# Performance work log

Hardware: AMD Instinct MI355X
Metric: run time of the kernel (lower is better)

Reference implementation:

```python
import jax, jax.numpy as jnp
import numpy as np

B, K, D_MODEL = 128, 256, 256
NUM_CODES, BASIS_DIM = 1024, 2700


def setup_inputs() -> dict:
    key = jax.random.key(0)
    k1, k2, k3 = jax.random.split(key, 3)
    slot_features = jax.random.normal(k1, (B, K, D_MODEL), dtype=jnp.float32)
    W_proj = jax.random.normal(k2, (BASIS_DIM, D_MODEL), dtype=jnp.float32) * 0.02
    b_proj = jnp.zeros((BASIS_DIM,), dtype=jnp.float32)
    # NMF basis atoms are non-negative
    basis = jax.random.uniform(k3, (NUM_CODES, BASIS_DIM), dtype=jnp.float32)
    return {"slot_features": slot_features, "W_proj": W_proj, "b_proj": b_proj, "basis": basis}


def reference(slot_features, W_proj, b_proj, basis):
    b, k, _ = slot_features.shape
    # slot_proj: Linear(d_model -> basis_dim)
    z_e = jnp.einsum('bkd,ed->bke', slot_features, W_proj) + b_proj  # [B,K,BASIS_DIM]
    z_flat = z_e.reshape(b * k, -1)                                   # [BK, D]
    # squared-euclidean distance to every codebook atom: [BK, NUM_CODES]
    dist = (jnp.sum(z_flat * z_flat, axis=1, keepdims=True)
            - 2.0 * (z_flat @ basis.T)
            + jnp.sum(basis * basis, axis=1)[None, :])
    indices = jnp.argmin(dist, axis=-1)                               # [BK]
    e_i = basis[indices].reshape(b, k, -1)                            # [B,K,D]
    # straight-through: forward value == z_e, grads pass through z_e only
    q_st = z_e + jax.lax.stop_gradient(e_i - z_e)
    commit_loss = jnp.mean((z_e - jax.lax.stop_gradient(e_i)) ** 2)
    vq_loss = 0.25 * commit_loss
    logits = -dist                                                    # [BK, NUM_CODES]
    avg_probs = jnp.mean(jax.nn.softmax(logits, axis=-1), axis=0)     # [NUM_CODES]
    entropy = -jnp.sum(avg_probs * jnp.log(avg_probs + 1e-8))
    return q_st, indices.reshape(b, k), vq_loss, entropy
```

## Files before the change

kernel.cpp:

```cpp
#include <hip/hip_runtime.h>
#include <math.h>

#define ED 2700
#define NC 1024
#define DM 256
#define BKROWS 32768

#define IDX_OFF 88473600
#define VQ_OFF  88506368
#define ENT_OFF 88506369

#define KPAD 2720
#define K2CH 8

typedef float  f32x4  __attribute__((ext_vector_type(4)));
typedef short  bf16x8 __attribute__((ext_vector_type(8)));

__device__ inline unsigned short f2bf(float x) {
    unsigned int u = __float_as_uint(x);
    unsigned int r = (u + 0x7FFFu + ((u >> 16) & 1u)) >> 16;
    return (unsigned short)r;
}
__device__ inline float bf2f(unsigned short h) {
    return __uint_as_float(((unsigned int)h) << 16);
}


__global__ __launch_bounds__(256)
void k_packS(const float* __restrict__ S, unsigned short* __restrict__ Sh,
             unsigned short* __restrict__ Sm) {
    const size_t i4 = (size_t)blockIdx.x * 256 + threadIdx.x;
    const float4 v = *(const float4*)(S + i4 * 4);
    ushort4 hv, mv;
    unsigned short* hp = (unsigned short*)&hv;
    unsigned short* mp = (unsigned short*)&mv;
    const float xs[4] = {v.x, v.y, v.z, v.w};
    #pragma unroll
    for (int j = 0; j < 4; ++j) {
        const unsigned short h = f2bf(xs[j]);
        hp[j] = h;
        mp[j] = f2bf(xs[j] - bf2f(h));
    }
    *(ushort4*)(Sh + i4 * 4) = hv;
    *(ushort4*)(Sm + i4 * 4) = mv;
}

__global__ void k_prepB(const float* __restrict__ basis, const float* __restrict__ bproj,
                        float* __restrict__ bP, float* __restrict__ bsq) {
    const int c = blockIdx.x;
    const int t = threadIdx.x;
    const float* row = basis + (size_t)c * ED;
    float* dst = bP + (size_t)c * KPAD;
    double s2 = 0.0, sp = 0.0;
    for (int j = t; j < ED; j += 256) {
        const float x = row[j];
        dst[j] = x;
        s2 += (double)x * (double)x;
        sp += (double)x * (double)bproj[j];
    }
    if (t < KPAD - ED) dst[ED + t] = 0.f;
    __shared__ double sd[512];
    sd[t] = s2; sd[256 + t] = sp;
    __syncthreads();
    for (int off = 128; off > 0; off >>= 1) {
        if (t < off) { sd[t] += sd[t + off]; sd[256 + t] += sd[256 + t + off]; }
        __syncthreads();
    }
    if (t == 0) bsq[c] = (float)(sd[0] - 2.0 * sd[256]);
}

__global__ __launch_bounds__(256)
void k_padWT(const float* __restrict__ W, float* __restrict__ WT) {
    const int e0 = blockIdx.x * 64;
    const int d0 = blockIdx.y * 64;
    __shared__ float tbuf[64][65];
    const int t  = threadIdx.x;
    const int r  = t >> 2;
    const int q4 = t & 3;
    #pragma unroll
    for (int j = 0; j < 4; ++j) {
        const int col = q4 * 16 + j * 4;
        const int e = e0 + r;
        float4 v = make_float4(0.f, 0.f, 0.f, 0.f);
        if (e < ED) v = *(const float4*)(W + (size_t)e * DM + d0 + col);
        tbuf[r][col + 0] = v.x; tbuf[r][col + 1] = v.y;
        tbuf[r][col + 2] = v.z; tbuf[r][col + 3] = v.w;
    }
    __syncthreads();
    #pragma unroll
    for (int j = 0; j < 4; ++j) {
        const int col = q4 * 16 + j * 4;
        if (e0 + col < KPAD) {
            float4 o;
            o.x = tbuf[col + 0][r]; o.y = tbuf[col + 1][r];
            o.z = tbuf[col + 2][r]; o.w = tbuf[col + 3][r];
            *(float4*)(WT + (size_t)(d0 + r) * KPAD + e0 + col) = o;
        }
    }
}

__global__ __launch_bounds__(256)
void k_uv2(const float* __restrict__ WT, const float* __restrict__ bproj,
           float* __restrict__ uv) {
    const int b = blockIdx.x;
    const int t = threadIdx.x;
    double s = 0.0;
    if (b < 256) {
        const float* row = WT + (size_t)b * KPAD;
        for (int j = t; j < ED; j += 256) s += (double)row[j] * (double)bproj[j];
    } else {
        for (int j = t; j < ED; j += 256) { const double x = bproj[j]; s += x * x; }
    }
    __shared__ double sd[256];
    sd[t] = s;
    __syncthreads();
    for (int off = 128; off > 0; off >>= 1) {
        if (t < off) sd[t] += sd[t + off];
        __syncthreads();
    }
    if (t == 0) uv[b] = (float)sd[0];
}

__global__ __launch_bounds__(256)
void k_colsum(const float* __restrict__ S, float* __restrict__ cspart) {
    const int m0 = blockIdx.x * 256;
    const int t  = threadIdx.x;
    double s = 0.0;
    for (int r = 0; r < 256; ++r) s += (double)S[(size_t)(m0 + r) * DM + t];
    cspart[blockIdx.x * 256 + t] = (float)s;
}

__global__ __launch_bounds__(256)
void k_gsplit(const float* __restrict__ A, const float* __restrict__ B,
              float* __restrict__ Cp, int nld) {
    const int n0  = blockIdx.x * 64;
    const int m0  = blockIdx.y * 64;
    const int k00 = blockIdx.z * 544;
    float* Cout = Cp + (size_t)blockIdx.z * (size_t)gridDim.y * 64 * nld;
    const int t  = threadIdx.x;
    const int tx = t & 15, ty = t >> 4;

    __shared__ float alds[32 * 68];
    __shared__ float blds[32 * 68];

    float acc[4][4] = {};

    for (int k0 = k00; k0 < k00 + 544; k0 += 32) {
        #pragma unroll
        for (int rep = 0; rep < 2; ++rep) {
            const int id  = t + rep * 256;
            const int row = id >> 3, kq = id & 7;
            const float4 va = *(const float4*)(A + (size_t)(m0 + row) * KPAD + k0 + 4 * kq);
            alds[(4*kq+0)*68 + row] = va.x;
            alds[(4*kq+1)*68 + row] = va.y;
            alds[(4*kq+2)*68 + row] = va.z;
            alds[(4*kq+3)*68 + row] = va.w;
            const float4 vb = *(const float4*)(B + (size_t)(n0 + row) * KPAD + k0 + 4 * kq);
            blds[(4*kq+0)*68 + row] = vb.x;
            blds[(4*kq+1)*68 + row] = vb.y;
            blds[(4*kq+2)*68 + row] = vb.z;
            blds[(4*kq+3)*68 + row] = vb.w;
        }
        __syncthreads();
        #pragma unroll 8
        for (int k = 0; k < 32; ++k) {
            const float4 a = *(const float4*)&alds[k*68 + 4*ty];
            const float4 b = *(const float4*)&blds[k*68 + 4*tx];
            const float av[4] = {a.x, a.y, a.z, a.w};
            const float bv[4] = {b.x, b.y, b.z, b.w};
            #pragma unroll
            for (int i = 0; i < 4; ++i)
                #pragma unroll
                for (int j = 0; j < 4; ++j)
                    acc[i][j] = fmaf(av[i], bv[j], acc[i][j]);
        }
        __syncthreads();
    }
    #pragma unroll
    for (int i = 0; i < 4; ++i) {
        float4 o; o.x = acc[i][0]; o.y = acc[i][1]; o.z = acc[i][2]; o.w = acc[i][3];
        *(float4*)(Cout + (size_t)(m0 + 4*ty + i) * nld + n0 + 4*tx) = o;
    }
}

__global__ __launch_bounds__(256)
void k_redP(const float* __restrict__ Pp, unsigned short* __restrict__ Ph,
            unsigned short* __restrict__ Pm) {
    const size_t idx = (size_t)blockIdx.x * 256 + threadIdx.x;
    float s = 0.f;
    #pragma unroll
    for (int k = 0; k < 5; ++k) s += Pp[(size_t)k * 262144 + idx];
    const unsigned short h = f2bf(s);
    Ph[idx] = h;
    Pm[idx] = f2bf(s - bf2f(h));
}

__global__ __launch_bounds__(256)
void k_redM2(const float* __restrict__ Mp, unsigned short* __restrict__ Mh,
             unsigned short* __restrict__ Mm) {
    const size_t idx = (size_t)blockIdx.x * 256 + threadIdx.x;
    float s = 0.f;
    #pragma unroll
    for (int k = 0; k < 5; ++k) s += Mp[(size_t)k * 65536 + idx];
    const unsigned short h = f2bf(s);
    Mh[idx] = h;
    Mm[idx] = f2bf(s - bf2f(h));
}

__global__ __launch_bounds__(512, 2)
void k_gemm2(const unsigned short* __restrict__ Zh, const unsigned short* __restrict__ Zm,
             const unsigned short* __restrict__ Bh, const unsigned short* __restrict__ Bm,
             float* __restrict__ G) {
    __shared__ unsigned short lds[2 * 32768];

    const int bid  = blockIdx.x;
    const int xcd  = bid & 7, local = bid >> 3;
    const int mt   = xcd * 16 + (local >> 2);
    const int nt   = local & 3;
    const int m0   = mt * 256, n0 = nt * 256;
    const int tid  = threadIdx.x;
    const int w    = tid >> 6, l = tid & 63;
    const int wr   = (w >> 2) * 128;
    const int wc   = (w & 3) * 64;
    const int lrow = l & 15;
    const int lu   = l >> 4;

    const unsigned short* hsrc[4][2];
    int hlds[4][2];
    #pragma unroll
    for (int ht = 0; ht < 4; ++ht) {
        #pragma unroll
        for (int j = 0; j < 2; ++j) {
            const int slot = j * 512 + tid;
            const int rwh  = slot >> 3;
            const int unit = slot & 7;
            int row; bool isB;
            if (ht == 0)      { row = (rwh & 63) + (rwh >> 6) * 128;       isB = false; }
            else if (ht == 1) { row = 64 + (rwh & 63) + (rwh >> 6) * 128;  isB = false; }
            else if (ht == 2) { row = (rwh & 31) + (rwh >> 5) * 64;        isB = true;  }
            else              { row = 32 + (rwh & 31) + (rwh >> 5) * 64;   isB = true;  }
            const int sg   = unit ^ (row & 7);
            const int pl   = sg >> 2;
            const int koff = (sg & 3) * 8;
            if (!isB) hsrc[ht][j] = (pl ? Zm : Zh) + (size_t)(m0 + row) * DM + koff;
            else      hsrc[ht][j] = (pl ? Bm : Bh) + (size_t)(n0 + row) * DM + koff;
            hlds[ht][j] = (isB ? 16384 : 0) + row * 64 + unit * 8;
        }
    }

    f32x4 acc[8][4];
    #pragma unroll
    for (int i = 0; i < 8; ++i)
        #pragma unroll
        for (int j = 0; j < 4; ++j) acc[i][j] = (f32x4){0.f, 0.f, 0.f, 0.f};

    #define STAGE_HALF(ht, ck, db) { \
        _Pragma("unroll") \
        for (int j = 0; j < 2; ++j) \
            __builtin_amdgcn_global_load_lds( \
                (const __attribute__((address_space(1))) unsigned int*)(const void*)(hsrc[ht][j] + (ck) * 32), \
                (__attribute__((address_space(3))) unsigned int*)(void*)&lds[(db) * 32768 + hlds[ht][j]], \
                16, 0, 0); \
    }

    #define LOAD_A(db, qm) { \
        const unsigned short* At = &lds[(db) * 32768]; \
        _Pragma("unroll") \
        for (int f = 0; f < 4; ++f) { \
            const int row = wr + ((qm) * 4 + f) * 16 + lrow; \
            ah[f] = *(const bf16x8*)(At + row * 64 + (((0 + lu) ^ (row & 7))) * 8); \
            am[f] = *(const bf16x8*)(At + row * 64 + (((4 + lu) ^ (row & 7))) * 8); \
        } \
    }
    #define LOAD_B(db, qn) { \
        const unsigned short* Bt = &lds[(db) * 32768 + 16384]; \
        _Pragma("unroll") \
        for (int f = 0; f < 2; ++f) { \
            const int col = wc + ((qn) * 2 + f) * 16 + lrow; \
            bh[f] = *(const bf16x8*)(Bt + col * 64 + (((0 + lu) ^ (col & 7))) * 8); \
            bm[f] = *(const bf16x8*)(Bt + col * 64 + (((4 + lu) ^ (col & 7))) * 8); \
        } \
    }
    #define MFMA_Q(qm, qn) { \
        __builtin_amdgcn_s_setprio(1); \
        _Pragma("unroll") \
        for (int i = 0; i < 4; ++i) \
            _Pragma("unroll") \
            for (int j = 0; j < 2; ++j) { \
                f32x4 cc = acc[(qm) * 4 + i][(qn) * 2 + j]; \
                cc = __builtin_amdgcn_mfma_f32_16x16x32_bf16(ah[i], bh[j], cc, 0, 0, 0); \
                cc = __builtin_amdgcn_mfma_f32_16x16x32_bf16(ah[i], bm[j], cc, 0, 0, 0); \
                cc = __builtin_amdgcn_mfma_f32_16x16x32_bf16(am[i], bh[j], cc, 0, 0, 0); \
                acc[(qm) * 4 + i][(qn) * 2 + j] = cc; \
            } \
        __builtin_amdgcn_s_setprio(0); \
    }
    #define VM8  asm volatile("s_waitcnt vmcnt(8)" ::: "memory");
    #define BAR  __builtin_amdgcn_s_barrier();

    STAGE_HALF(0, 0, 0) STAGE_HALF(2, 0, 0) STAGE_HALF(3, 0, 0) STAGE_HALF(1, 0, 0)
    STAGE_HALF(0, 1, 1) STAGE_HALF(2, 1, 1)
    VM8
    BAR

    for (int c = 0; c < K2CH - 2; ++c) {
        const int cb = c & 1, ob = cb ^ 1;
        bf16x8 ah[4], am[4], bh[2], bm[2];
        LOAD_A(cb, 0) LOAD_B(cb, 0)
        STAGE_HALF(3, c + 1, ob)
        BAR
        MFMA_Q(0, 0)
        VM8
        BAR
        LOAD_B(cb, 1)
        STAGE_HALF(1, c + 1, ob)
        BAR
        MFMA_Q(0, 1)
        VM8
        BAR
        LOAD_A(cb, 1) LOAD_B(cb, 0)
        STAGE_HALF(0, c + 2, cb)
        BAR
        MFMA_Q(1, 0)
        BAR
        LOAD_B(cb, 1)
        STAGE_HALF(2, c + 2, cb)
        BAR
        MFMA_Q(1, 1)
        VM8
        BAR
    }

    STAGE_HALF(3, K2CH - 1, (K2CH - 1) & 1) STAGE_HALF(1, K2CH - 1, (K2CH - 1) & 1)
    asm volatile("s_waitcnt vmcnt(0)" ::: "memory");
    BAR
    #pragma unroll
    for (int e = 0; e < 2; ++e) {
        const int cb = (K2CH - 2 + e) & 1;
        bf16x8 ah[4], am[4], bh[2], bm[2];
        LOAD_A(cb, 0) LOAD_B(cb, 0)
        MFMA_Q(0, 0)
        LOAD_B(cb, 1)
        MFMA_Q(0, 1)
        LOAD_A(cb, 1) LOAD_B(cb, 0)
        MFMA_Q(1, 0)
        LOAD_B(cb, 1)
        MFMA_Q(1, 1)
    }

    #pragma unroll
    for (int fm = 0; fm < 8; ++fm)
        #pragma unroll
        for (int fn = 0; fn < 4; ++fn) {
            const int col = n0 + wc + fn * 16 + lrow;
            #pragma unroll
            for (int r = 0; r < 4; ++r) {
                const int row = m0 + wr + fm * 16 + lu * 4 + r;
                G[(size_t)row * NC + col] = acc[fm][fn][r];
            }
        }
}

__global__ __launch_bounds__(512, 2)
void k_ydot(const unsigned short* __restrict__ Zh, const unsigned short* __restrict__ Zm,
            const unsigned short* __restrict__ Bh, const unsigned short* __restrict__ Bm,
            const float* __restrict__ S, float* __restrict__ ydotpart) {
    __shared__ unsigned short lds[2 * 32768];

    const int bid  = blockIdx.x;
    const int xcd  = bid & 7, local = bid >> 3;
    const int mt   = xcd * 16 + local;
    const int m0   = mt * 256, n0 = 0;
    const int tid  = threadIdx.x;
    const int w    = tid >> 6, l = tid & 63;
    const int wr   = (w >> 2) * 128;
    const int wc   = (w & 3) * 64;
    const int lrow = l & 15;
    const int lu   = l >> 4;

    const unsigned short* hsrc[4][2];
    int hlds[4][2];
    #pragma unroll
    for (int ht = 0; ht < 4; ++ht) {
        #pragma unroll
        for (int j = 0; j < 2; ++j) {
            const int slot = j * 512 + tid;
            const int rwh  = slot >> 3;
            const int unit = slot & 7;
            int row; bool isB;
            if (ht == 0)      { row = (rwh & 63) + (rwh >> 6) * 128;       isB = false; }
            else if (ht == 1) { row = 64 + (rwh & 63) + (rwh >> 6) * 128;  isB = false; }
            else if (ht == 2) { row = (rwh & 31) + (rwh >> 5) * 64;        isB = true;  }
            else              { row = 32 + (rwh & 31) + (rwh >> 5) * 64;   isB = true;  }
            const int sg   = unit ^ (row & 7);
            const int pl   = sg >> 2;
            const int koff = (sg & 3) * 8;
            if (!isB) hsrc[ht][j] = (pl ? Zm : Zh) + (size_t)(m0 + row) * DM + koff;
            else      hsrc[ht][j] = (pl ? Bm : Bh) + (size_t)(n0 + row) * DM + koff;
            hlds[ht][j] = (isB ? 16384 : 0) + row * 64 + unit * 8;
        }
    }

    f32x4 acc[8][4];
    #pragma unroll
    for (int i = 0; i < 8; ++i)
        #pragma unroll
        for (int j = 0; j < 4; ++j) acc[i][j] = (f32x4){0.f, 0.f, 0.f, 0.f};

    STAGE_HALF(0, 0, 0) STAGE_HALF(2, 0, 0) STAGE_HALF(3, 0, 0) STAGE_HALF(1, 0, 0)
    STAGE_HALF(0, 1, 1) STAGE_HALF(2, 1, 1)
    VM8
    BAR

    for (int c = 0; c < K2CH - 2; ++c) {
        const int cb = c & 1, ob = cb ^ 1;
        bf16x8 ah[4], am[4], bh[2], bm[2];
        LOAD_A(cb, 0) LOAD_B(cb, 0)
        STAGE_HALF(3, c + 1, ob)
        BAR
        MFMA_Q(0, 0)
        VM8
        BAR
        LOAD_B(cb, 1)
        STAGE_HALF(1, c + 1, ob)
        BAR
        MFMA_Q(0, 1)
        VM8
        BAR
        LOAD_A(cb, 1) LOAD_B(cb, 0)
        STAGE_HALF(0, c + 2, cb)
        BAR
        MFMA_Q(1, 0)
        BAR
        LOAD_B(cb, 1)
        STAGE_HALF(2, c + 2, cb)
        BAR
        MFMA_Q(1, 1)
        VM8
        BAR
    }

    STAGE_HALF(3, K2CH - 1, (K2CH - 1) & 1) STAGE_HALF(1, K2CH - 1, (K2CH - 1) & 1)
    asm volatile("s_waitcnt vmcnt(0)" ::: "memory");
    BAR
    #pragma unroll
    for (int e = 0; e < 2; ++e) {
        const int cb = (K2CH - 2 + e) & 1;
        bf16x8 ah[4], am[4], bh[2], bm[2];
        LOAD_A(cb, 0) LOAD_B(cb, 0)
        MFMA_Q(0, 0)
        LOAD_B(cb, 1)
        MFMA_Q(0, 1)
        LOAD_A(cb, 1) LOAD_B(cb, 0)
        MFMA_Q(1, 0)
        LOAD_B(cb, 1)
        MFMA_Q(1, 1)
    }
    #undef STAGE_HALF
    #undef LOAD_A
    #undef LOAD_B
    #undef MFMA_Q
    #undef VM8
    #undef BAR

    float part = 0.f;
    #pragma unroll
    for (int fm = 0; fm < 8; ++fm)
        #pragma unroll
        for (int fn = 0; fn < 4; ++fn) {
            const int col = wc + fn * 16 + lrow;
            #pragma unroll
            for (int r = 0; r < 4; ++r) {
                const int row = m0 + wr + fm * 16 + lu * 4 + r;
                part += acc[fm][fn][r] * S[(size_t)row * DM + col];
            }
        }
    __syncthreads();
    float* red = (float*)lds;
    red[tid] = part;
    __syncthreads();
    for (int off = 256; off > 0; off >>= 1) {
        if (tid < off) red[tid] += red[tid + off];
        __syncthreads();
    }
    if (tid == 0) ydotpart[bid] = red[0];
}

__global__ __launch_bounds__(512)
void k_post(const float* __restrict__ G, const float* __restrict__ bsq,
            float* __restrict__ A, float* __restrict__ wgpart,
            int* __restrict__ idxws, float* __restrict__ out) {
    const int bid = blockIdx.x;
    const int wr0 = bid * 32;
    const int t   = threadIdx.x;
    const int cg  = t & 127;
    const int rq  = t >> 7;
    const int r0  = rq * 8;
    const int c0  = cg * 4;
    const int c1  = 512 + cg * 4;

    __shared__ float sm[9280];
    float* red_v    = sm;
    int*   red_i    = (int*)(sm + 4096);
    float* row_dmin = sm + 8192;
    float* row_s    = sm + 8224;
    float* pc       = sm + 8256;

    float acc[8][8];
    #pragma unroll
    for (int i = 0; i < 8; ++i) {
        const float4 g0 = *(const float4*)&G[(size_t)(wr0 + r0 + i) * NC + c0];
        const float4 g1 = *(const float4*)&G[(size_t)(wr0 + r0 + i) * NC + c1];
        acc[i][0] = g0.x; acc[i][1] = g0.y; acc[i][2] = g0.z; acc[i][3] = g0.w;
        acc[i][4] = g1.x; acc[i][5] = g1.y; acc[i][6] = g1.z; acc[i][7] = g1.w;
    }

    float bsqv[8];
    #pragma unroll
    for (int j = 0; j < 4; ++j) { bsqv[j] = bsq[c0 + j]; bsqv[4 + j] = bsq[c1 + j]; }

    #pragma unroll
    for (int i = 0; i < 8; ++i)
        #pragma unroll
        for (int j = 0; j < 8; ++j)
            acc[i][j] = bsqv[j] - 2.f * acc[i][j];

    #pragma unroll
    for (int i = 0; i < 8; ++i) {
        float bv = acc[i][0]; int bi = c0;
        #pragma unroll
        for (int j = 1; j < 8; ++j) {
            const int c = (j < 4) ? (c0 + j) : (c1 + (j - 4));
            if (acc[i][j] < bv || (acc[i][j] == bv && c < bi)) { bv = acc[i][j]; bi = c; }
        }
        red_v[(r0 + i) * 128 + cg] = bv;
        red_i[(r0 + i) * 128 + cg] = bi;
    }
    __syncthreads();
    if (t < 32) {
        float bv = red_v[t * 128]; int bi = red_i[t * 128];
        for (int x = 1; x < 128; ++x) {
            const float v = red_v[t * 128 + x];
            const int  iv = red_i[t * 128 + x];
            if (v < bv || (v == bv && iv < bi)) { bv = v; bi = iv; }
        }
        row_dmin[t] = bv;
        idxws[wr0 + t] = bi;
        out[IDX_OFF + wr0 + t] = (float)bi;
    }
    __syncthreads();

    float su[8];
    #pragma unroll
    for (int i = 0; i < 8; ++i) {
        const float dm = row_dmin[r0 + i];
        float s = 0.f;
        #pragma unroll
        for (int j = 0; j < 8; ++j) {
            const float u = expf(dm - acc[i][j]);
            acc[i][j] = u;
            s += u;
        }
        su[i] = s;
    }
    #pragma unroll
    for (int i = 0; i < 8; ++i) red_v[(r0 + i) * 128 + cg] = su[i];
    __syncthreads();
    if (t < 32) {
        float s = 0.f;
        for (int x = 0; x < 128; ++x) s += red_v[t * 128 + x];
        row_s[t] = s;
    }
    __syncthreads();

    float rcp[8];
    #pragma unroll
    for (int i = 0; i < 8; ++i) rcp[i] = 1.f / row_s[r0 + i];

    pc[t] = 0.f; pc[t + 512] = 0.f;
    __syncthreads();
    #pragma unroll
    for (int j = 0; j < 8; ++j) {
        const int c = (j < 4) ? (c0 + j) : (c1 + (j - 4));
        float s = 0.f;
        #pragma unroll
        for (int i = 0; i < 8; ++i) s += acc[i][j] * rcp[i];
        atomicAdd(&pc[c], s);
    }
    __syncthreads();
    atomicAdd(&A[t],       pc[t]);
    atomicAdd(&A[t + 512], pc[t + 512]);

    if (t == 0) {
        float s = 0.f;
        for (int r = 0; r < 32; ++r) s += row_dmin[r];
        wgpart[bid] = s;
    }
}

__global__ void k_final2(const float* __restrict__ wgpart, const float* __restrict__ Aq,
                         const float* __restrict__ ydotpart, const float* __restrict__ cspart,
                         const float* __restrict__ uv, float* __restrict__ out) {
    __shared__ double sd[1024];
    const int t = threadIdx.x;
    sd[t] = (double)wgpart[t];
    __syncthreads();
    for (int off = 512; off > 0; off >>= 1) {
        if (t < off) sd[t] += sd[t + off];
        __syncthreads();
    }
    const double smin = sd[0];
    __syncthreads();
    sd[t] = (t < 128) ? (double)ydotpart[t] : 0.0;
    __syncthreads();
    for (int off = 512; off > 0; off >>= 1) {
        if (t < off) sd[t] += sd[t + off];
        __syncthreads();
    }
    const double sy = sd[0];
    __syncthreads();
    double cu = 0.0;
    if (t < 256) {
        double cs = 0.0;
        for (int b = 0; b < 128; ++b) cs += (double)cspart[b * 256 + t];
        cu = cs * (double)uv[t];
    }
    sd[t] = cu;
    __syncthreads();
    for (int off = 512; off > 0; off >>= 1) {
        if (t < off) sd[t] += sd[t + off];
        __syncthreads();
    }
    if (t == 0) {
        const double szsq = sy + 2.0 * sd[0] + 32768.0 * (double)uv[256];
        out[VQ_OFF] = (float)(0.25 * (smin + szsq) / 88473600.0);
    }
    __syncthreads();
    const double p = (double)Aq[t] * (1.0 / 32768.0);
    sd[t] = -p * log(p + 1e-8);
    __syncthreads();
    for (int off = 512; off > 0; off >>= 1) {
        if (t < off) sd[t] += sd[t + off];
        __syncthreads();
    }
    if (t == 0) out[ENT_OFF] = (float)sd[0];
}

__global__ void k_gather(const float* __restrict__ basis, const int* __restrict__ idxws,
                         float* __restrict__ out) {
    const int r = blockIdx.x;
    const int idx = idxws[r];
    const float4* src = (const float4*)(basis + (size_t)idx * ED);
    float4* dst = (float4*)(out + (size_t)r * ED);
    for (int j = threadIdx.x; j < ED / 4; j += 256) dst[j] = src[j];
}


__global__ void k_bsq(const float* __restrict__ basis, float* __restrict__ bsq) {
    int c = blockIdx.x;
    const float* row = basis + (size_t)c * ED;
    double s = 0.0;
    for (int j = threadIdx.x; j < ED; j += 256) { float v = row[j]; s += (double)v * (double)v; }
    __shared__ double sd[256];
    sd[threadIdx.x] = s;
    __syncthreads();
    for (int off = 128; off > 0; off >>= 1) {
        if (threadIdx.x < off) sd[threadIdx.x] += sd[threadIdx.x + off];
        __syncthreads();
    }
    if (threadIdx.x == 0) bsq[c] = (float)sd[0];
}

__global__ __launch_bounds__(256, 4)
void k_gemm1(const float* __restrict__ S, const float* __restrict__ W,
             const float* __restrict__ bproj, float* __restrict__ Z) {
    const int e0 = blockIdx.x * 64;
    const int m0 = blockIdx.y * 64;
    const int t  = threadIdx.x;
    const int tx = t & 15, ty = t >> 4;
    __shared__ float alds[32 * 68];
    __shared__ float blds[32 * 68];
    float acc[4][4] = {};
    for (int k0 = 0; k0 < DM; k0 += 32) {
        #pragma unroll
        for (int rep = 0; rep < 2; ++rep) {
            const int id  = t + rep * 256;
            const int row = id >> 3, kq = id & 7;
            const float4 va = *(const float4*)(S + (size_t)(m0 + row) * DM + k0 + 4 * kq);
            alds[(4*kq+0)*68 + row] = va.x;
            alds[(4*kq+1)*68 + row] = va.y;
            alds[(4*kq+2)*68 + row] = va.z;
            alds[(4*kq+3)*68 + row] = va.w;
            float4 vb = make_float4(0.f, 0.f, 0.f, 0.f);
            if (e0 + row < ED)
                vb = *(const float4*)(W + (size_t)(e0 + row) * DM + k0 + 4 * kq);
            blds[(4*kq+0)*68 + row] = vb.x;
            blds[(4*kq+1)*68 + row] = vb.y;
            blds[(4*kq+2)*68 + row] = vb.z;
            blds[(4*kq+3)*68 + row] = vb.w;
        }
        __syncthreads();
        #pragma unroll 8
        for (int k = 0; k < 32; ++k) {
            const float4 a = *(const float4*)&alds[k*68 + 4*ty];
            const float4 b = *(const float4*)&blds[k*68 + 4*tx];
            const float av[4] = {a.x, a.y, a.z, a.w};
            const float bv[4] = {b.x, b.y, b.z, b.w};
            #pragma unroll
            for (int i = 0; i < 4; ++i)
                #pragma unroll
                for (int j = 0; j < 4; ++j)
                    acc[i][j] = fmaf(av[i], bv[j], acc[i][j]);
        }
        __syncthreads();
    }
    const bool valid = (e0 + 4*tx + 4) <= ED;
    float4 bias = make_float4(0.f, 0.f, 0.f, 0.f);
    if (valid) bias = *(const float4*)(bproj + e0 + 4*tx);
    #pragma unroll
    for (int i = 0; i < 4; ++i) {
        if (valid) {
            float4 o;
            o.x = acc[i][0] + bias.x;
            o.y = acc[i][1] + bias.y;
            o.z = acc[i][2] + bias.z;
            o.w = acc[i][3] + bias.w;
            *(float4*)(Z + (size_t)(m0 + 4*ty + i) * ED + e0 + 4*tx) = o;
        }
    }
}

__global__ __launch_bounds__(64)
void k_zsq(const float* __restrict__ Z, float* __restrict__ zsq) {
    const int r = blockIdx.x;
    const float4* row4 = (const float4*)(Z + (size_t)r * ED);
    double s = 0.0;
    for (int q = threadIdx.x; q < ED / 4; q += 64) {
        const float4 v = row4[q];
        s += (double)v.x * v.x + (double)v.y * v.y + (double)v.z * v.z + (double)v.w * v.w;
    }
    #pragma unroll
    for (int off = 32; off > 0; off >>= 1) s += __shfl_down(s, off);
    if (threadIdx.x == 0) zsq[r] = (float)s;
}

__global__ __launch_bounds__(512, 2)
void k_dist(const float* __restrict__ Z, const float* __restrict__ basis,
            const float* __restrict__ bsq, const float* __restrict__ zsq,
            float* __restrict__ A, float* __restrict__ wgpart,
            int* __restrict__ idxws, float* __restrict__ out) {
    const int bid = blockIdx.x;
    const int wr0 = bid * 32;
    const int t   = threadIdx.x;
    const int cg  = t & 127;
    const int rq  = t >> 7;
    const int r0  = rq * 8;
    const int c0  = cg * 4;
    const int c1  = 512 + cg * 4;
    __shared__ float blds[16 * 1024];
    __shared__ float zlds[16 * 36];
    float acc[8][8];
    #pragma unroll
    for (int i = 0; i < 8; ++i)
        #pragma unroll
        for (int j = 0; j < 8; ++j) acc[i][j] = 0.f;
    for (int k0 = 0; k0 < ED; k0 += 16) {
        const bool full = (k0 + 16) <= ED;
        #pragma unroll
        for (int rep = 0; rep < 2; ++rep) {
            const int c = t + rep * 512;
            const float* bp = basis + (size_t)c * ED + k0;
            if (full) {
                const float4 v0 = *(const float4*)(bp + 0);
                const float4 v1 = *(const float4*)(bp + 4);
                const float4 v2 = *(const float4*)(bp + 8);
                const float4 v3 = *(const float4*)(bp + 12);
                blds[ 0*1024+c]=v0.x; blds[ 1*1024+c]=v0.y; blds[ 2*1024+c]=v0.z; blds[ 3*1024+c]=v0.w;
                blds[ 4*1024+c]=v1.x; blds[ 5*1024+c]=v1.y; blds[ 6*1024+c]=v1.z; blds[ 7*1024+c]=v1.w;
                blds[ 8*1024+c]=v2.x; blds[ 9*1024+c]=v2.y; blds[10*1024+c]=v2.z; blds[11*1024+c]=v2.w;
                blds[12*1024+c]=v3.x; blds[13*1024+c]=v3.y; blds[14*1024+c]=v3.z; blds[15*1024+c]=v3.w;
            } else {
                for (int kk = 0; kk < 16; ++kk)
                    blds[kk*1024 + c] = (k0 + kk < ED) ? bp[kk] : 0.f;
            }
        }
        if (t < 128) {
            const int row = t >> 2, kq = t & 3;
            const float* zp = Z + (size_t)(wr0 + row) * ED + k0 + 4 * kq;
            if (full) {
                const float4 v = *(const float4*)zp;
                zlds[(4*kq+0)*36 + row] = v.x;
                zlds[(4*kq+1)*36 + row] = v.y;
                zlds[(4*kq+2)*36 + row] = v.z;
                zlds[(4*kq+3)*36 + row] = v.w;
            } else {
                for (int j = 0; j < 4; ++j) {
                    const int k = k0 + 4*kq + j;
                    zlds[(4*kq+j)*36 + row] = (k < ED) ? zp[j] : 0.f;
                }
            }
        }
        __syncthreads();
        #pragma unroll
        for (int k = 0; k < 16; ++k) {
            const float4 z0 = *(const float4*)&zlds[k*36 + r0];
            const float4 z1 = *(const float4*)&zlds[k*36 + r0 + 4];
            const float4 b0 = *(const float4*)&blds[k*1024 + c0];
            const float4 b1 = *(const float4*)&blds[k*1024 + c1];
            const float zz[8] = {z0.x, z0.y, z0.z, z0.w, z1.x, z1.y, z1.z, z1.w};
            const float bb[8] = {b0.x, b0.y, b0.z, b0.w, b1.x, b1.y, b1.z, b1.w};
            #pragma unroll
            for (int i = 0; i < 8; ++i)
                #pragma unroll
                for (int j = 0; j < 8; ++j)
                    acc[i][j] = fmaf(zz[i], bb[j], acc[i][j]);
        }
        __syncthreads();
    }
    float* red_v    = blds;
    int*   red_i    = (int*)(blds + 4096);
    float* row_dmin = blds + 8192;
    float* row_s    = blds + 8224;
    float* pc       = blds + 8256;
    float bsqv[8], zsqv[8];
    #pragma unroll
    for (int j = 0; j < 4; ++j) { bsqv[j] = bsq[c0 + j]; bsqv[4 + j] = bsq[c1 + j]; }
    #pragma unroll
    for (int i = 0; i < 8; ++i) zsqv[i] = zsq[wr0 + r0 + i];
    #pragma unroll
    for (int i = 0; i < 8; ++i)
        #pragma unroll
        for (int j = 0; j < 8; ++j) {
            const float tv = zsqv[i] - 2.f * acc[i][j];
            acc[i][j] = tv + bsqv[j];
        }
    #pragma unroll
    for (int i = 0; i < 8; ++i) {
        float bv = acc[i][0]; int bi = c0;
        #pragma unroll
        for (int j = 1; j < 8; ++j) {
            const int c = (j < 4) ? (c0 + j) : (c1 + (j - 4));
            if (acc[i][j] < bv || (acc[i][j] == bv && c < bi)) { bv = acc[i][j]; bi = c; }
        }
        red_v[(r0 + i) * 128 + cg] = bv;
        red_i[(r0 + i) * 128 + cg] = bi;
    }
    __syncthreads();
    if (t < 32) {
        float bv = red_v[t * 128]; int bi = red_i[t * 128];
        for (int x = 1; x < 128; ++x) {
            const float v = red_v[t * 128 + x];
            const int  iv = red_i[t * 128 + x];
            if (v < bv || (v == bv && iv < bi)) { bv = v; bi = iv; }
        }
        row_dmin[t] = bv;
        idxws[wr0 + t] = bi;
        out[IDX_OFF + wr0 + t] = (float)bi;
    }
    __syncthreads();
    float su[8];
    #pragma unroll
    for (int i = 0; i < 8; ++i) {
        const float dm = row_dmin[r0 + i];
        float s = 0.f;
        #pragma unroll
        for (int j = 0; j < 8; ++j) {
            const float u = expf(dm - acc[i][j]);
            acc[i][j] = u;
            s += u;
        }
        su[i] = s;
    }
    #pragma unroll
    for (int i = 0; i < 8; ++i) red_v[(r0 + i) * 128 + cg] = su[i];
    __syncthreads();
    if (t < 32) {
        float s = 0.f;
        for (int x = 0; x < 128; ++x) s += red_v[t * 128 + x];
        row_s[t] = s;
    }
    __syncthreads();
    float rcp[8];
    #pragma unroll
    for (int i = 0; i < 8; ++i) rcp[i] = 1.f / row_s[r0 + i];
    pc[t] = 0.f; pc[t + 512] = 0.f;
    __syncthreads();
    #pragma unroll
    for (int j = 0; j < 8; ++j) {
        const int c = (j < 4) ? (c0 + j) : (c1 + (j - 4));
        float s = 0.f;
        #pragma unroll
        for (int i = 0; i < 8; ++i) s += acc[i][j] * rcp[i];
        atomicAdd(&pc[c], s);
    }
    __syncthreads();
    atomicAdd(&A[t],       pc[t]);
    atomicAdd(&A[t + 512], pc[t + 512]);
    if (t == 0) {
        float s = 0.f;
        for (int r = 0; r < 32; ++r) s += row_dmin[r];
        wgpart[bid] = s;
    }
}

__global__ void k_final(const float* __restrict__ wgpart, const float* __restrict__ A,
                        float* __restrict__ out) {
    __shared__ double sd[1024];
    const int t = threadIdx.x;
    sd[t] = (double)wgpart[t];
    __syncthreads();
    for (int off = 512; off > 0; off >>= 1) {
        if (t < off) sd[t] += sd[t + off];
        __syncthreads();
    }
    if (t == 0) out[VQ_OFF] = (float)(0.25 * sd[0] / 88473600.0);
    __syncthreads();
    const double p = (double)A[t] * (1.0 / 32768.0);
    sd[t] = -p * log(p + 1e-8);
    __syncthreads();
    for (int off = 512; off > 0; off >>= 1) {
        if (t < off) sd[t] += sd[t + off];
        __syncthreads();
    }
    if (t == 0) out[ENT_OFF] = (float)sd[0];
}


extern "C" void kernel_launch(void* const* d_in, const int* in_sizes, int n_in,
                              void* d_out, int out_size, void* d_ws, size_t ws_size,
                              hipStream_t stream) {
    const float* S     = (const float*)d_in[0];
    const float* W     = (const float*)d_in[1];
    const float* bproj = (const float*)d_in[2];
    const float* basis = (const float*)d_in[3];
    float* out = (float*)d_out;
    float* ws  = (float*)d_ws;

    const size_t NEED = (size_t)33951232 * sizeof(float);
    if (ws_size >= NEED) {
        float* A        = ws;
        float* bsq      = ws + 1024;
        float* wgpart   = ws + 2048;
        int*   idxws    = (int*)(ws + 3072);
        float* uv       = ws + 35840;
        float* ydotpart = ws + 36224;
        float* cspart   = ws + 36352;
        unsigned short* Ph = (unsigned short*)(ws + 69120);
        unsigned short* Pm = (unsigned short*)(ws + 200192);
        unsigned short* Mh = (unsigned short*)(ws + 331264);
        unsigned short* Mm = (unsigned short*)(ws + 364032);
        float* G        = ws + 396800;
        float* basisP = G;
        float* WT     = G + 2785280;
        float* Pp     = G + 3481600;
        float* Mp     = G + 4792320;
        unsigned short* Sh = (unsigned short*)out;
        unsigned short* Sm = Sh + (size_t)BKROWS * DM;

        hipMemsetAsync(A, 0, (size_t)NC * sizeof(float), stream);
        k_packS <<<BKROWS * DM / 1024, 256, 0, stream>>>(S, Sh, Sm);
        k_prepB <<<NC, 256, 0, stream>>>(basis, bproj, basisP, bsq);
        k_padWT <<<dim3(43, 4), 256, 0, stream>>>(W, WT);
        k_uv2   <<<257, 256, 0, stream>>>(WT, bproj, uv);
        k_colsum<<<128, 256, 0, stream>>>(S, cspart);
        k_gsplit<<<dim3(4, 16, 5), 256, 0, stream>>>(basisP, WT, Pp, 256);
        k_gsplit<<<dim3(4, 4, 5),  256, 0, stream>>>(WT, WT, Mp, 256);
        k_redP  <<<1024, 256, 0, stream>>>(Pp, Ph, Pm);
        k_redM2 <<<256, 256, 0, stream>>>(Mp, Mh, Mm);
        k_gemm2 <<<512, 512, 0, stream>>>(Sh, Sm, Ph, Pm, G);
        k_ydot  <<<128, 512, 0, stream>>>(Sh, Sm, Mh, Mm, S, ydotpart);
        k_post  <<<BKROWS / 32, 512, 0, stream>>>(G, bsq, A, wgpart, idxws, out);
        k_final2<<<1, 1024, 0, stream>>>(wgpart, A, ydotpart, cspart, uv, out);
        k_gather<<<BKROWS, 256, 0, stream>>>(basis, idxws, out);
    } else {
        float* zsqF    = ws;
        float* A       = ws + 32768;
        float* bsqF    = ws + 33792;
        float* wgpartF = ws + 34816;
        int*   idxwsF  = (int*)(ws + 35840);
        float* Z = out;
        hipMemsetAsync(A, 0, (size_t)NC * sizeof(float), stream);
        k_bsq   <<<NC, 256, 0, stream>>>(basis, bsqF);
        k_gemm1 <<<dim3(43, 512), 256, 0, stream>>>(S, W, bproj, Z);
        k_zsq   <<<BKROWS, 64, 0, stream>>>(Z, zsqF);
        k_dist  <<<BKROWS / 32, 512, 0, stream>>>(Z, basis, bsqF, zsqF, A, wgpartF, idxwsF, out);
        k_final <<<1, 1024, 0, stream>>>(wgpartF, A, out);
        k_gather<<<BKROWS, 256, 0, stream>>>(basis, idxwsF, out);
    }
}
```

Before: 367.6 us.

## Merge prep kernels into one launch and fuse codebook gather into post kernel

Combines the basis prep, W transpose, uv, and column-sum kernels into one multi-role launch. It also merges the two split-K GEMMs and the two reductions into single launches. The gather of selected codebook rows moves into the post/argmin kernel, dropping the index workspace round trip and a separate launch. This cuts launch overhead and lets independent small kernels run concurrently. The cost is that each post block now does extra serial copying, and uv now reads W with strided loads.

```diff
diff --git a/kernel.cpp b/kernel.cpp
--- a/kernel.cpp
+++ b/kernel.cpp
@@ -45,98 +45,108 @@
     *(ushort4*)(Sm + i4 * 4) = mv;
 }
 
-__global__ void k_prepB(const float* __restrict__ basis, const float* __restrict__ bproj,
-                        float* __restrict__ bP, float* __restrict__ bsq) {
-    const int c = blockIdx.x;
-    const int t = threadIdx.x;
-    const float* row = basis + (size_t)c * ED;
-    float* dst = bP + (size_t)c * KPAD;
-    double s2 = 0.0, sp = 0.0;
-    for (int j = t; j < ED; j += 256) {
-        const float x = row[j];
-        dst[j] = x;
-        s2 += (double)x * (double)x;
-        sp += (double)x * (double)bproj[j];
-    }
-    if (t < KPAD - ED) dst[ED + t] = 0.f;
-    __shared__ double sd[512];
-    sd[t] = s2; sd[256 + t] = sp;
-    __syncthreads();
-    for (int off = 128; off > 0; off >>= 1) {
-        if (t < off) { sd[t] += sd[t + off]; sd[256 + t] += sd[256 + t + off]; }
-        __syncthreads();
-    }
-    if (t == 0) bsq[c] = (float)(sd[0] - 2.0 * sd[256]);
-}
-
 __global__ __launch_bounds__(256)
-void k_padWT(const float* __restrict__ W, float* __restrict__ WT) {
-    const int e0 = blockIdx.x * 64;
-    const int d0 = blockIdx.y * 64;
-    __shared__ float tbuf[64][65];
-    const int t  = threadIdx.x;
-    const int r  = t >> 2;
-    const int q4 = t & 3;
-    #pragma unroll
-    for (int j = 0; j < 4; ++j) {
-        const int col = q4 * 16 + j * 4;
-        const int e = e0 + r;
-        float4 v = make_float4(0.f, 0.f, 0.f, 0.f);
-        if (e < ED) v = *(const float4*)(W + (size_t)e * DM + d0 + col);
-        tbuf[r][col + 0] = v.x; tbuf[r][col + 1] = v.y;
-        tbuf[r][col + 2] = v.z; tbuf[r][col + 3] = v.w;
-    }
-    __syncthreads();
-    #pragma unroll
-    for (int j = 0; j < 4; ++j) {
-        const int col = q4 * 16 + j * 4;
-        if (e0 + col < KPAD) {
-            float4 o;
-            o.x = tbuf[col + 0][r]; o.y = tbuf[col + 1][r];
-            o.z = tbuf[col + 2][r]; o.w = tbuf[col + 3][r];
-            *(float4*)(WT + (size_t)(d0 + r) * KPAD + e0 + col) = o;
-        }
-    }
-}
-
-__global__ __launch_bounds__(256)
-void k_uv2(const float* __restrict__ WT, const float* __restrict__ bproj,
-           float* __restrict__ uv) {
+void k_prep1(const float* __restrict__ basis, const float* __restrict__ bproj,
+             const float* __restrict__ W, const float* __restrict__ S,
+             float* __restrict__ bP, float* __restrict__ bsq,
+             float* __restrict__ WT, float* __restrict__ uv,
+             float* __restrict__ cspart) {
+    __shared__ double sdbuf[2080];
     const int b = blockIdx.x;
     const int t = threadIdx.x;
-    double s = 0.0;
-    if (b < 256) {
-        const float* row = WT + (size_t)b * KPAD;
-        for (int j = t; j < ED; j += 256) s += (double)row[j] * (double)bproj[j];
+
+    if (b < 1024) {
+        const int c = b;
+        const float* row = basis + (size_t)c * ED;
+        float* dst = bP + (size_t)c * KPAD;
+        double s2 = 0.0, sp = 0.0;
+        for (int j = t; j < ED; j += 256) {
+            const float x = row[j];
+            dst[j] = x;
+            s2 += (double)x * (double)x;
+            sp += (double)x * (double)bproj[j];
+        }
+        if (t < KPAD - ED) dst[ED + t] = 0.f;
+        double* sd = sdbuf;
+        sd[t] = s2; sd[256 + t] = sp;
+        __syncthreads();
+        for (int off = 128; off > 0; off >>= 1) {
+            if (t < off) { sd[t] += sd[t + off]; sd[256 + t] += sd[256 + t + off]; }
+            __syncthreads();
+        }
+        if (t == 0) bsq[c] = (float)(sd[0] - 2.0 * sd[256]);
+    } else if (b < 1196) {
+        const int i  = b - 1024;
+        const int e0 = (i >> 2) * 64;
+        const int d0 = (i & 3) * 64;
+        float (*tbuf)[65] = (float(*)[65])sdbuf;
+        const int r  = t >> 2;
+        const int q4 = t & 3;
+        #pragma unroll
+        for (int j = 0; j < 4; ++j) {
+            const int col = q4 * 16 + j * 4;
+            const int e = e0 + r;
+            float4 v = make_float4(0.f, 0.f, 0.f, 0.f);
+            if (e < ED) v = *(const float4*)(W + (size_t)e * DM + d0 + col);
+            tbuf[r][col + 0] = v.x; tbuf[r][col + 1] = v.y;
+            tbuf[r][col + 2] = v.z; tbuf[r][col + 3] = v.w;
+        }
+        __syncthreads();
+        #pragma unroll
+        for (int j = 0; j < 4; ++j) {
+            const int col = q4 * 16 + j * 4;
+            if (e0 + col < KPAD) {
+                float4 o;
+                o.x = tbuf[col + 0][r]; o.y = tbuf[col + 1][r];
+                o.z = tbuf[col + 2][r]; o.w = tbuf[col + 3][r];
+                *(float4*)(WT + (size_t)(d0 + r) * KPAD + e0 + col) = o;
+            }
+        }
+    } else if (b < 1453) {
+        const int bb = b - 1196;
+        double s = 0.0;
+        if (bb < 256) {
+            for (int e = t; e < ED; e += 256)
+                s += (double)W[(size_t)e * DM + bb] * (double)bproj[e];
+        } else {
+            for (int j = t; j < ED; j += 256) { const double x = bproj[j]; s += x * x; }
+        }
+        double* sd = sdbuf;
+        sd[t] = s;
+        __syncthreads();
+        for (int off = 128; off > 0; off >>= 1) {
+            if (t < off) sd[t] += sd[t + off];
+            __syncthreads();
+        }
+        if (t == 0) uv[bb] = (float)sd[0];
     } else {
-        for (int j = t; j < ED; j += 256) { const double x = bproj[j]; s += x * x; }
-    }
-    __shared__ double sd[256];
-    sd[t] = s;
-    __syncthreads();
-    for (int off = 128; off > 0; off >>= 1) {
-        if (t < off) sd[t] += sd[t + off];
-        __syncthreads();
-    }
-    if (t == 0) uv[b] = (float)sd[0];
+        const int m0 = (b - 1453) * 256;
+        double s = 0.0;
+        for (int r = 0; r < 256; ++r) s += (double)S[(size_t)(m0 + r) * DM + t];
+        cspart[(b - 1453) * 256 + t] = (float)s;
+    }
 }
 
 __global__ __launch_bounds__(256)
-void k_colsum(const float* __restrict__ S, float* __restrict__ cspart) {
-    const int m0 = blockIdx.x * 256;
-    const int t  = threadIdx.x;
-    double s = 0.0;
-    for (int r = 0; r < 256; ++r) s += (double)S[(size_t)(m0 + r) * DM + t];
-    cspart[blockIdx.x * 256 + t] = (float)s;
-}
-
-__global__ __launch_bounds__(256)
-void k_gsplit(const float* __restrict__ A, const float* __restrict__ B,
-              float* __restrict__ Cp, int nld) {
-    const int n0  = blockIdx.x * 64;
-    const int m0  = blockIdx.y * 64;
-    const int k00 = blockIdx.z * 544;
-    float* Cout = Cp + (size_t)blockIdx.z * (size_t)gridDim.y * 64 * nld;
+void k_gsplitPM(const float* __restrict__ basisP, const float* __restrict__ WT,
+                float* __restrict__ Pp, float* __restrict__ Mp) {
+    const int b = blockIdx.x;
+    const float* A;
+    const float* B = WT;
+    float* Cout;
+    int n0, m0, k00, mtiles;
+    if (b < 320) {
+        const int kz = b / 64, rem = b % 64;
+        A = basisP; mtiles = 16;
+        m0 = (rem >> 2) * 64; n0 = (rem & 3) * 64; k00 = kz * 544;
+        Cout = Pp + (size_t)kz * mtiles * 64 * 256;
+    } else {
+        const int j = b - 320;
+        const int kz = j / 16, rem = j % 16;
+        A = WT; mtiles = 4;
+        m0 = (rem >> 2) * 64; n0 = (rem & 3) * 64; k00 = kz * 544;
+        Cout = Mp + (size_t)kz * mtiles * 64 * 256;
+    }
     const int t  = threadIdx.x;
     const int tx = t & 15, ty = t >> 4;
 
@@ -165,9 +175,9 @@
         #pragma unroll 8
         for (int k = 0; k < 32; ++k) {
             const float4 a = *(const float4*)&alds[k*68 + 4*ty];
-            const float4 b = *(const float4*)&blds[k*68 + 4*tx];
+            const float4 bb = *(const float4*)&blds[k*68 + 4*tx];
             const float av[4] = {a.x, a.y, a.z, a.w};
-            const float bv[4] = {b.x, b.y, b.z, b.w};
+            const float bv[4] = {bb.x, bb.y, bb.z, bb.w};
             #pragma unroll
             for (int i = 0; i < 4; ++i)
                 #pragma unroll
@@ -179,32 +189,32 @@
     #pragma unroll
     for (int i = 0; i < 4; ++i) {
         float4 o; o.x = acc[i][0]; o.y = acc[i][1]; o.z = acc[i][2]; o.w = acc[i][3];
-        *(float4*)(Cout + (size_t)(m0 + 4*ty + i) * nld + n0 + 4*tx) = o;
+        *(float4*)(Cout + (size_t)(m0 + 4*ty + i) * 256 + n0 + 4*tx) = o;
     }
 }
 
 __global__ __launch_bounds__(256)
-void k_redP(const float* __restrict__ Pp, unsigned short* __restrict__ Ph,
-            unsigned short* __restrict__ Pm) {
-    const size_t idx = (size_t)blockIdx.x * 256 + threadIdx.x;
-    float s = 0.f;
-    #pragma unroll
-    for (int k = 0; k < 5; ++k) s += Pp[(size_t)k * 262144 + idx];
-    const unsigned short h = f2bf(s);
-    Ph[idx] = h;
-    Pm[idx] = f2bf(s - bf2f(h));
-}
-
-__global__ __launch_bounds__(256)
-void k_redM2(const float* __restrict__ Mp, unsigned short* __restrict__ Mh,
-             unsigned short* __restrict__ Mm) {
-    const size_t idx = (size_t)blockIdx.x * 256 + threadIdx.x;
-    float s = 0.f;
-    #pragma unroll
-    for (int k = 0; k < 5; ++k) s += Mp[(size_t)k * 65536 + idx];
-    const unsigned short h = f2bf(s);
-    Mh[idx] = h;
-    Mm[idx] = f2bf(s - bf2f(h));
+void k_redPM(const float* __restrict__ Pp, const float* __restrict__ Mp,
+             unsigned short* __restrict__ Ph, unsigned short* __restrict__ Pm,
+             unsigned short* __restrict__ Mh, unsigned short* __restrict__ Mm) {
+    const int b = blockIdx.x;
+    if (b < 1024) {
+        const size_t idx = (size_t)b * 256 + threadIdx.x;
+        float s = 0.f;
+        #pragma unroll
+        for (int k = 0; k < 5; ++k) s += Pp[(size_t)k * 262144 + idx];
+        const unsigned short h = f2bf(s);
+        Ph[idx] = h;
+        Pm[idx] = f2bf(s - bf2f(h));
+    } else {
+        const size_t idx = (size_t)(b - 1024) * 256 + threadIdx.x;
+        float s = 0.f;
+        #pragma unroll
+        for (int k = 0; k < 5; ++k) s += Mp[(size_t)k * 65536 + idx];
+        const unsigned short h = f2bf(s);
+        Mh[idx] = h;
+        Mm[idx] = f2bf(s - bf2f(h));
+    }
 }
 
 __global__ __launch_bounds__(512, 2)
@@ -487,9 +497,9 @@
 }
 
 __global__ __launch_bounds__(512)
-void k_post(const float* __restrict__ G, const float* __restrict__ bsq,
-            float* __restrict__ A, float* __restrict__ wgpart,
-            int* __restrict__ idxws, float* __restrict__ out) {
+void k_postg(const float* __restrict__ G, const float* __restrict__ bsq,
+             const float* __restrict__ basis, float* __restrict__ A,
+             float* __restrict__ wgpart, float* __restrict__ out) {
     const int bid = blockIdx.x;
     const int wr0 = bid * 32;
     const int t   = threadIdx.x;
@@ -499,12 +509,13 @@
     const int c0  = cg * 4;
     const int c1  = 512 + cg * 4;
 
-    __shared__ float sm[9280];
+    __shared__ float sm[9312];
     float* red_v    = sm;
     int*   red_i    = (int*)(sm + 4096);
     float* row_dmin = sm + 8192;
     float* row_s    = sm + 8224;
-    float* pc       = sm + 8256;
+    int*   idxsh    = (int*)(sm + 8256);
+    float* pc       = sm + 8288;
 
     float acc[8][8];
     #pragma unroll
@@ -545,7 +556,7 @@
             if (v < bv || (v == bv && iv < bi)) { bv = v; bi = iv; }
         }
         row_dmin[t] = bv;
-        idxws[wr0 + t] = bi;
+        idxsh[t] = bi;
         out[IDX_OFF + wr0 + t] = (float)bi;
     }
     __syncthreads();
@@ -595,6 +606,13 @@
         float s = 0.f;
         for (int r = 0; r < 32; ++r) s += row_dmin[r];
         wgpart[bid] = s;
+    }
+
+    for (int r = 0; r < 32; ++r) {
+        const int idx = idxsh[r];
+        const float4* src = (const float4*)(basis + (size_t)idx * ED);
+        float4* dst = (float4*)(out + (size_t)(wr0 + r) * ED);
+        for (int j = t; j < ED / 4; j += 512) dst[j] = src[j];
     }
 }
 
@@ -941,7 +959,6 @@
         float* A        = ws;
         float* bsq      = ws + 1024;
         float* wgpart   = ws + 2048;
-        int*   idxws    = (int*)(ws + 3072);
         float* uv       = ws + 35840;
         float* ydotpart = ws + 36224;
         float* cspart   = ws + 36352;
@@ -958,20 +975,14 @@
         unsigned short* Sm = Sh + (size_t)BKROWS * DM;
 
         hipMemsetAsync(A, 0, (size_t)NC * sizeof(float), stream);
-        k_packS <<<BKROWS * DM / 1024, 256, 0, stream>>>(S, Sh, Sm);
-        k_prepB <<<NC, 256, 0, stream>>>(basis, bproj, basisP, bsq);
-        k_padWT <<<dim3(43, 4), 256, 0, stream>>>(W, WT);
-        k_uv2   <<<257, 256, 0, stream>>>(WT, bproj, uv);
-        k_colsum<<<128, 256, 0, stream>>>(S, cspart);
-        k_gsplit<<<dim3(4, 16, 5), 256, 0, stream>>>(basisP, WT, Pp, 256);
-        k_gsplit<<<dim3(4, 4, 5),  256, 0, stream>>>(WT, WT, Mp, 256);
-        k_redP  <<<1024, 256, 0, stream>>>(Pp, Ph, Pm);
-        k_redM2 <<<256, 256, 0, stream>>>(Mp, Mh, Mm);
-        k_gemm2 <<<512, 512, 0, stream>>>(Sh, Sm, Ph, Pm, G);
-        k_ydot  <<<128, 512, 0, stream>>>(Sh, Sm, Mh, Mm, S, ydotpart);
-        k_post  <<<BKROWS / 32, 512, 0, stream>>>(G, bsq, A, wgpart, idxws, out);
-        k_final2<<<1, 1024, 0, stream>>>(wgpart, A, ydotpart, cspart, uv, out);
-        k_gather<<<BKROWS, 256, 0, stream>>>(basis, idxws, out);
+        k_packS   <<<BKROWS * DM / 1024, 256, 0, stream>>>(S, Sh, Sm);
+        k_prep1   <<<1581, 256, 0, stream>>>(basis, bproj, W, S, basisP, bsq, WT, uv, cspart);
+        k_gsplitPM<<<400, 256, 0, stream>>>(basisP, WT, Pp, Mp);
+        k_redPM   <<<1280, 256, 0, stream>>>(Pp, Mp, Ph, Pm, Mh, Mm);
+        k_gemm2   <<<512, 512, 0, stream>>>(Sh, Sm, Ph, Pm, G);
+        k_ydot    <<<128, 512, 0, stream>>>(Sh, Sm, Mh, Mm, S, ydotpart);
+        k_postg   <<<BKROWS / 32, 512, 0, stream>>>(G, bsq, basis, A, wgpart, out);
+        k_final2  <<<1, 1024, 0, stream>>>(wgpart, A, ydotpart, cspart, uv, out);
     } else {
         float* zsqF    = ws;
         float* A       = ws + 32768;
```

New measurement: 326.1 us. -11.3%, faster.
